# Optimization experiments

Hardware: AMD Instinct MI355X
Metric: run time of the kernel (lower is better)

The kernel has to match this reference:

```python
import jax, jax.numpy as jnp
import numpy as np

N = 50000
E = 800000
NFEAT = 128
NHID = 64
NCLASS = 40


def setup_inputs() -> dict:
    key = jax.random.key(0)
    ks = jax.random.split(key, 12)
    return {
        "x": jax.random.normal(ks[0], (N, NFEAT), dtype=jnp.float32),
        "M": jax.random.uniform(ks[1], (N, 1), dtype=jnp.float32),
        "AM": jax.random.uniform(ks[2], (N, 1), dtype=jnp.float32),
        "adj_vals": jax.random.uniform(ks[3], (E,), dtype=jnp.float32),
        "adjZ_vals": jax.random.uniform(ks[4], (E,), dtype=jnp.float32),
        "W0": jax.random.normal(ks[5], (NFEAT, NFEAT), dtype=jnp.float32) * (1.414 / np.sqrt(NFEAT)),
        "b0": jnp.zeros((NFEAT,), dtype=jnp.float32),
        "W1": jax.random.normal(ks[6], (NFEAT, NHID), dtype=jnp.float32) * (1.414 / np.sqrt(NFEAT)),
        "b1": jnp.zeros((NHID,), dtype=jnp.float32),
        "W2": jax.random.normal(ks[7], (NHID, NCLASS), dtype=jnp.float32) * (1.0 / np.sqrt(NHID)),
        "b2": jnp.zeros((NCLASS,), dtype=jnp.float32),
        "row": jax.random.randint(ks[8], (E,), 0, N, dtype=jnp.int32),
        "col": jax.random.randint(ks[9], (E,), 0, N, dtype=jnp.int32),
    }


def _spmm(vals, row, col, X, n):
    # sparse (COO) @ dense: out[r] = sum_e vals[e] * X[col[e]] for row[e]==r
    return jax.ops.segment_sum(vals[:, None] * X[col], row, num_segments=n)


def reference(x, M, AM, adj_vals, adjZ_vals, W0, b0, W1, b1, W2, b2, row, col):
    n = x.shape[0]
    # gc0: PaGConv(nfeat->nfeat) on adjZ, then ReLU (dropout is identity in eval)
    h = _spmm(adjZ_vals, row, col, M * x, n) * AM
    h = jax.nn.relu(h @ W0 + b0)
    # gc1: PaGConv(nfeat->nhid) on adjZ, then ReLU
    h = _spmm(adjZ_vals, row, col, M * h, n) * AM
    h = jax.nn.relu(h @ W1 + b1)
    # gc2: plain GConv(nhid->nclass) on adj
    h = _spmm(adj_vals, row, col, h, n)
    h = h @ W2 + b2
    return jax.nn.log_softmax(h, axis=1)
```

## Files before the change

### kernel.cpp

```cpp
#include <hip/hip_runtime.h>
#include <hip/hip_bf16.h>
#include <math.h>


typedef __attribute__((ext_vector_type(8))) short bf16x8;
typedef __attribute__((ext_vector_type(4))) float f32x4;

#define HIST_EPB_LOG 14
#define HIST_EPB 16384
#define NBINS 50176

__device__ __forceinline__ float rl_f(float v, int j) {
    return __builtin_bit_cast(float,
        __builtin_amdgcn_readlane(__builtin_bit_cast(int, v), j));
}
__device__ __forceinline__ int rl_i(int v, int j) {
    return __builtin_amdgcn_readlane(v, j);
}
__device__ __forceinline__ unsigned short f2bf(float f) {
    unsigned u = __builtin_bit_cast(unsigned, f);
    u += 0x7fffu + ((u >> 16) & 1u);
    return (unsigned short)(u >> 16);
}
__device__ __forceinline__ unsigned pack2bf(float lo, float hi) {
    return (unsigned)f2bf(lo) | ((unsigned)f2bf(hi) << 16);
}
__device__ __forceinline__ float bf_lo(unsigned u) {
    return __builtin_bit_cast(float, u << 16);
}
__device__ __forceinline__ float bf_hi(unsigned u) {
    return __builtin_bit_cast(float, u & 0xffff0000u);
}
__device__ __forceinline__ float clampf(float v) {
    return fminf(fmaxf(v, -1e30f), 1e30f);
}


__global__ void prep_wt(const float* __restrict__ W0, const float* __restrict__ W1,
                        const float* __restrict__ W2,
                        unsigned short* __restrict__ wt0, unsigned short* __restrict__ wt1,
                        unsigned short* __restrict__ wt2) {
    int idx = blockIdx.x * 256 + threadIdx.x;
    if (idx < 128 * 128) {
        int nn = idx >> 7, k = idx & 127;
        wt0[idx] = f2bf(W0[k * 128 + nn]);
    }
    idx -= 128 * 128;
    if (idx >= 0 && idx < 64 * 128) {
        int nn = idx >> 7, k = idx & 127;
        wt1[idx] = f2bf(W1[k * 64 + nn]);
    }
    idx -= 64 * 128;
    if (idx >= 0 && idx < 48 * 64) {
        int nn = idx >> 6, k = idx & 63;
        wt2[idx] = (nn < 40) ? f2bf(W2[k * 40 + nn]) : (unsigned short)0;
    }
}


template <int K, int COLS, int NTPAD, bool ABF16, bool MSCALE>
__device__ __forceinline__ void gemm_mfma_body(const void* __restrict__ Asrc,
                                               const float* __restrict__ Mv,
                                               const unsigned short* __restrict__ Wt,
                                               unsigned short* __restrict__ outp,
                                               int n, int bid, int tid) {
    constexpr int KS = K / 32;
    const int lane = tid & 63;
    const int wid = tid >> 6;
    const int m15 = lane & 15;
    const int q = lane >> 4;
    const int rA = bid * 64 + wid * 16 + m15;

    bf16x8 a[KS];
    if constexpr (ABF16) {
        const unsigned short* A = (const unsigned short*)Asrc;
#pragma unroll
        for (int ks = 0; ks < KS; ++ks) {
            uint4 z = make_uint4(0u, 0u, 0u, 0u);
            if (rA < n) z = *(const uint4*)(A + (size_t)rA * K + ks * 32 + q * 8);
            a[ks] = __builtin_bit_cast(bf16x8, z);
        }
    } else {
        const float* A = (const float*)Asrc;
        float m = 1.0f;
        if constexpr (MSCALE) { if (rA < n) m = Mv[rA]; }
#pragma unroll
        for (int ks = 0; ks < KS; ++ks) {
            float4 lo = make_float4(0.f, 0.f, 0.f, 0.f);
            float4 hi = make_float4(0.f, 0.f, 0.f, 0.f);
            if (rA < n) {
                lo = *(const float4*)(A + (size_t)rA * K + ks * 32 + q * 8);
                hi = *(const float4*)(A + (size_t)rA * K + ks * 32 + q * 8 + 4);
            }
            union { bf16x8 v; unsigned short u[8]; } pk;
            pk.u[0] = f2bf(lo.x * m); pk.u[1] = f2bf(lo.y * m);
            pk.u[2] = f2bf(lo.z * m); pk.u[3] = f2bf(lo.w * m);
            pk.u[4] = f2bf(hi.x * m); pk.u[5] = f2bf(hi.y * m);
            pk.u[6] = f2bf(hi.z * m); pk.u[7] = f2bf(hi.w * m);
            a[ks] = pk.v;
        }
    }

#pragma unroll
    for (int nt = 0; nt < NTPAD / 16; ++nt) {
        f32x4 acc = {0.f, 0.f, 0.f, 0.f};
        const int bn = nt * 16 + m15;
#pragma unroll
        for (int ks = 0; ks < KS; ++ks) {
            const uint4 z = *(const uint4*)(Wt + (size_t)bn * K + ks * 32 + q * 8);
            const bf16x8 b = __builtin_bit_cast(bf16x8, z);
            acc = __builtin_amdgcn_mfma_f32_16x16x32_bf16(a[ks], b, acc, 0, 0, 0);
        }
        const int gc = nt * 16 + m15;
#pragma unroll
        for (int rr = 0; rr < 4; ++rr) {
            const int gr = bid * 64 + wid * 16 + q * 4 + rr;
            bool ok = gr < n;
            if constexpr (NTPAD != COLS) ok = ok && (gc < COLS);
            if (ok) outp[(size_t)gr * COLS + gc] = f2bf(clampf(acc[rr]));
        }
    }
}

template <int K, int COLS, int NTPAD, bool ABF16, bool MSCALE>
__launch_bounds__(256)
__global__ void gemm_mfma(const void* __restrict__ A, const float* __restrict__ Mv,
                          const unsigned short* __restrict__ Wt,
                          unsigned short* __restrict__ out, int n) {
    gemm_mfma_body<K, COLS, NTPAD, ABF16, MSCALE>(A, Mv, Wt, out, n, blockIdx.x,
                                                  threadIdx.x);
}


__launch_bounds__(1024)
__global__ void hist_gemm0(const int* __restrict__ row,
                           unsigned short* __restrict__ cntmat,
                           unsigned short* __restrict__ lrank, int E, int NB,
                           const float* __restrict__ x, const float* __restrict__ Mv,
                           const unsigned short* __restrict__ Wt0,
                           unsigned short* __restrict__ t_buf, int n) {
    __shared__ unsigned hcnt[NBINS / 2];
    const int blk = blockIdx.x;
    const int t = threadIdx.x;
    if (blk < NB) {
        for (int i = t; i < NBINS / 2; i += 1024) hcnt[i] = 0u;
        __syncthreads();
        const int s = blk << HIST_EPB_LOG;
        const int e = min(E, s + HIST_EPB);
        for (int i = s + t; i < e; i += 1024) {
            const int r = row[i];
            const unsigned sh = (unsigned)(r & 1) << 4;
            const unsigned old = atomicAdd(&hcnt[r >> 1], 1u << sh);
            lrank[i] = (unsigned short)((old >> sh) & 0xffffu);
        }
        __syncthreads();
        unsigned* dst = (unsigned*)(cntmat + (size_t)blk * NBINS);
        for (int i = t; i < NBINS / 2; i += 1024) dst[i] = hcnt[i];
    } else {
        const int sub = t >> 8;
        gemm_mfma_body<128, 128, 128, false, true>(x, Mv, Wt0, t_buf, n,
                                                   (blk - NB) * 4 + sub, t & 255);
    }
}


__global__ void scan_sum(const unsigned short* __restrict__ cm, int* __restrict__ rp,
                         int* __restrict__ bsums, int n, int NB) {
    __shared__ int sdata[256];
    const int t = threadIdx.x;
    const int base = blockIdx.x * 1024 + t * 4;
    unsigned s0 = 0, s1 = 0, s2 = 0, s3 = 0;
    for (int b = 0; b < NB; ++b) {
        const uint2 c = *(const uint2*)&cm[(size_t)b * NBINS + base];
        s0 += c.x & 0xffffu; s1 += c.x >> 16;
        s2 += c.y & 0xffffu; s3 += c.y >> 16;
    }
    int v[4] = {(int)s0, (int)s1, (int)s2, (int)s3};
    const int tsum = v[0] + v[1] + v[2] + v[3];
    sdata[t] = tsum;
    __syncthreads();
    for (int off = 1; off < 256; off <<= 1) {
        int xv = (t >= off) ? sdata[t - off] : 0;
        __syncthreads();
        sdata[t] += xv;
        __syncthreads();
    }
    int run = sdata[t] - tsum;
    if (t == 255) bsums[blockIdx.x] = sdata[t];
#pragma unroll
    for (int i = 0; i < 4; ++i) {
        if (base + i < n) rp[base + i] = run;
        run += v[i];
    }
}


__launch_bounds__(256)
__global__ void scan_fin(const unsigned short* __restrict__ cm,
                         unsigned* __restrict__ cmabs, int* __restrict__ rp,
                         const int* __restrict__ bsums, int n, int NB, int E) {
    const int lane = threadIdx.x & 63;
    const int myblk = blockIdx.x >> 2;
    int bv = (lane < myblk) ? bsums[lane] : 0;
#pragma unroll
    for (int off = 32; off; off >>= 1) bv += __shfl_xor(bv, off);
    const int i = blockIdx.x * 256 + threadIdx.x;
    if (i < n) {
        int run = rp[i] + bv;
        rp[i] = run;
        for (int b = 0; b < NB; ++b) {
            cmabs[(size_t)b * NBINS + i] = (unsigned)run;
            run += (int)cm[(size_t)b * NBINS + i];
        }
    }
    if (blockIdx.x == 0 && threadIdx.x == 0) rp[n] = E;
}


__global__ void scatter_kernel(const int* __restrict__ row, const int* __restrict__ col,
                               const float* __restrict__ vA, const float* __restrict__ vZ,
                               const unsigned* __restrict__ cmabs,
                               const unsigned short* __restrict__ lrank,
                               float* __restrict__ packed, int E) {
    int e = blockIdx.x * blockDim.x + threadIdx.x;
    if (e >= E) return;
    const int r = row[e];
    const int pos = (int)(cmabs[(size_t)(e >> HIST_EPB_LOG) * NBINS + r]
                          + (unsigned)lrank[e]);
    float3 pk;
    pk.x = __int_as_float(col[e]);
    pk.y = vZ[e];
    pk.z = vA[e];
    *(float3*)&packed[(size_t)3 * pos] = pk;
}


__launch_bounds__(256)
__global__ void spmm128_kernel(const float* __restrict__ packed,
                               const int* __restrict__ rp, const unsigned short* __restrict__ X,
                               const float* __restrict__ AM, const float* __restrict__ Mv,
                               const float* __restrict__ bias,
                               unsigned short* __restrict__ out, int n) {
    const int lane = threadIdx.x & 63;
    const int r = (int)((blockIdx.x * (unsigned)blockDim.x + threadIdx.x) >> 6);
    if (r >= n) return;
    const int s = __builtin_amdgcn_readfirstlane(rp[r]);
    const int e = __builtin_amdgcn_readfirstlane(rp[r + 1]);

    float acc0 = 0.0f, acc1 = 0.0f;
    for (int base = s; base < e; base += 64) {
        const int nn = min(64, e - base);
        int ci = 0; float vf = 0.0f;
        if (lane < nn) {
            const float3 pk = *(const float3*)&packed[(size_t)3 * (base + lane)];
            ci = __builtin_bit_cast(int, pk.x);
            vf = pk.y;
        }
        int j = 0;
        for (; j + 16 <= nn; j += 16) {
            unsigned u[16];
#pragma unroll
            for (int q = 0; q < 16; ++q) {
                const int cq = rl_i(ci, j + q);
                u[q] = *(const unsigned*)(X + (size_t)cq * 128 + lane * 2);
            }
#pragma unroll
            for (int q = 0; q < 16; ++q) {
                const float vq = rl_f(vf, j + q);
                acc0 += vq * bf_lo(u[q]);
                acc1 += vq * bf_hi(u[q]);
            }
        }
        for (; j + 8 <= nn; j += 8) {
            unsigned u[8];
#pragma unroll
            for (int q = 0; q < 8; ++q) {
                const int cq = rl_i(ci, j + q);
                u[q] = *(const unsigned*)(X + (size_t)cq * 128 + lane * 2);
            }
#pragma unroll
            for (int q = 0; q < 8; ++q) {
                const float vq = rl_f(vf, j + q);
                acc0 += vq * bf_lo(u[q]);
                acc1 += vq * bf_hi(u[q]);
            }
        }
        for (; j < nn; ++j) {
            const int cq = rl_i(ci, j);
            const float vq = rl_f(vf, j);
            const unsigned u = *(const unsigned*)(X + (size_t)cq * 128 + lane * 2);
            acc0 += vq * bf_lo(u);
            acc1 += vq * bf_hi(u);
        }
    }

    const float am = AM[r];
    const float mr = Mv[r];
    const float o0 = fminf(fmaxf((acc0 * am + bias[2 * lane]) * mr, 0.0f), 1e30f);
    const float o1 = fminf(fmaxf((acc1 * am + bias[2 * lane + 1]) * mr, 0.0f), 1e30f);
    ((unsigned*)out)[(size_t)r * 64 + lane] = pack2bf(o0, o1);
}


__launch_bounds__(256)
__global__ void spmm64_kernel(const float* __restrict__ packed,
                              const int* __restrict__ rp, const unsigned short* __restrict__ X,
                              const float* __restrict__ AM, const float* __restrict__ bias,
                              unsigned short* __restrict__ out, int n) {
    const int lane = threadIdx.x & 63;
    const int g = lane >> 4;
    const int ls = lane & 15;
    const int r = (int)((blockIdx.x * (unsigned)blockDim.x + threadIdx.x) >> 6);
    if (r >= n) return;
    const int s = __builtin_amdgcn_readfirstlane(rp[r]);
    const int e = __builtin_amdgcn_readfirstlane(rp[r + 1]);

    float a0 = 0.0f, a1 = 0.0f, a2 = 0.0f, a3 = 0.0f;
    for (int base = s; base < e; base += 64) {
        const int nn = min(64, e - base);
        int ci = 0; float vf = 0.0f;
        if (lane < nn) {
            const float3 pk = *(const float3*)&packed[(size_t)3 * (base + lane)];
            ci = __builtin_bit_cast(int, pk.x);
            vf = pk.y;
        }
        for (int j = 0; j < nn; j += 16) {
#pragma unroll
            for (int q = 0; q < 4; ++q) {
                const int jj = j + 4 * q + g;
                const bool ok = jj < nn;
                const int idx = jj & 63;
                const int c = __shfl(ci, idx);
                const float v = __shfl(vf, idx);
                if (ok) {
                    const uint2 u = *(const uint2*)(X + (size_t)c * 64 + ls * 4);
                    a0 += v * bf_lo(u.x);
                    a1 += v * bf_hi(u.x);
                    a2 += v * bf_lo(u.y);
                    a3 += v * bf_hi(u.y);
                }
            }
        }
    }
    a0 += __shfl_xor(a0, 16); a0 += __shfl_xor(a0, 32);
    a1 += __shfl_xor(a1, 16); a1 += __shfl_xor(a1, 32);
    a2 += __shfl_xor(a2, 16); a2 += __shfl_xor(a2, 32);
    a3 += __shfl_xor(a3, 16); a3 += __shfl_xor(a3, 32);

    if (lane < 16) {
        const float am = AM[r];
        const float o0 = fminf(fmaxf(a0 * am + bias[4 * ls + 0], 0.0f), 1e30f);
        const float o1 = fminf(fmaxf(a1 * am + bias[4 * ls + 1], 0.0f), 1e30f);
        const float o2 = fminf(fmaxf(a2 * am + bias[4 * ls + 2], 0.0f), 1e30f);
        const float o3 = fminf(fmaxf(a3 * am + bias[4 * ls + 3], 0.0f), 1e30f);
        uint2 w;
        w.x = pack2bf(o0, o1);
        w.y = pack2bf(o2, o3);
        *(uint2*)((unsigned*)out + (size_t)r * 32 + ls * 2) = w;
    }
}


__launch_bounds__(256)
__global__ void spmm40_kernel(const float* __restrict__ packed,
                              const int* __restrict__ rp, const unsigned short* __restrict__ X,
                              const float* __restrict__ bias,
                              float* __restrict__ out, int n) {
    const int lane = threadIdx.x & 63;
    const int g = lane / 20;
    const int ls = lane - 20 * g;
    const bool active = g < 3;
    const int r = (int)((blockIdx.x * (unsigned)blockDim.x + threadIdx.x) >> 6);
    if (r >= n) return;
    const int s = __builtin_amdgcn_readfirstlane(rp[r]);
    const int e = __builtin_amdgcn_readfirstlane(rp[r + 1]);

    float acc0 = 0.0f, acc1 = 0.0f;
    for (int base = s; base < e; base += 64) {
        const int nn = min(64, e - base);
        int ci = 0; float vf = 0.0f;
        if (lane < nn) {
            const float3 pk = *(const float3*)&packed[(size_t)3 * (base + lane)];
            ci = __builtin_bit_cast(int, pk.x);
            vf = pk.z;
        }
        for (int j = 0; j < nn; j += 24) {
#pragma unroll
            for (int q = 0; q < 8; ++q) {
                const int jj = j + 3 * q + g;
                const bool ok = active && jj < nn;
                const int idx = jj & 63;
                const int c = __shfl(ci, idx);
                const float v = __shfl(vf, idx);
                if (ok) {
                    const unsigned u = *(const unsigned*)(X + (size_t)c * 40 + ls * 2);
                    acc0 += v * bf_lo(u);
                    acc1 += v * bf_hi(u);
                }
            }
        }
    }
    {
        const float a1 = __shfl(acc0, (lane + 20) & 63);
        const float a2 = __shfl(acc0, (lane + 40) & 63);
        const float b1 = __shfl(acc1, (lane + 20) & 63);
        const float b2 = __shfl(acc1, (lane + 40) & 63);
        acc0 += a1 + a2;
        acc1 += b1 + b2;
    }

    const bool own = lane < 20;
    const float vv0 = own ? fminf(fmaxf(acc0 + bias[2 * ls], -1e30f), 1e30f) : -INFINITY;
    const float vv1 = own ? fminf(fmaxf(acc1 + bias[2 * ls + 1], -1e30f), 1e30f) : -INFINITY;
    float mx = fmaxf(vv0, vv1);
#pragma unroll
    for (int off = 32; off > 0; off >>= 1) mx = fmaxf(mx, __shfl_xor(mx, off));
    float sum = own ? (expf(vv0 - mx) + expf(vv1 - mx)) : 0.0f;
#pragma unroll
    for (int off = 32; off > 0; off >>= 1) sum += __shfl_xor(sum, off);
    if (own) {
        const float lse = mx + logf(sum);
        *(float2*)(out + (size_t)r * 40 + ls * 2) = make_float2(vv0 - lse, vv1 - lse);
    }
}


extern "C" void kernel_launch(void* const* d_in, const int* in_sizes, int n_in,
                              void* d_out, int out_size, void* d_ws, size_t ws_size,
                              hipStream_t stream) {
    const float* x    = (const float*)d_in[0];
    const float* M    = (const float*)d_in[1];
    const float* AM   = (const float*)d_in[2];
    const float* adjv = (const float*)d_in[3];
    const float* adjZ = (const float*)d_in[4];
    const float* W0   = (const float*)d_in[5];
    const float* b0   = (const float*)d_in[6];
    const float* W1   = (const float*)d_in[7];
    const float* b1   = (const float*)d_in[8];
    const float* W2   = (const float*)d_in[9];
    const float* b2   = (const float*)d_in[10];
    const int* row    = (const int*)d_in[11];
    const int* col    = (const int*)d_in[12];
    float* out = (float*)d_out;

    const int n = in_sizes[1];
    const int E = in_sizes[3];

    float* t_f   = (float*)d_ws;
    unsigned short* t_buf = (unsigned short*)t_f;
    unsigned short* wt0 = t_buf + (size_t)n * 128;
    unsigned short* wt1 = wt0 + 128 * 128;
    unsigned short* wt2 = wt1 + 64 * 128;
    float* h_f   = t_f + (size_t)n * 128;
    unsigned short* h_buf = (unsigned short*)h_f;
    unsigned short* lrank  = (unsigned short*)h_f;
    unsigned short* cntmat = lrank + (size_t)E;
    unsigned* cmabs = (unsigned*)(cntmat + (size_t)64 * NBINS);
    int* rp      = (int*)(h_f + (size_t)n * 128);
    int* bsums   = rp + (n + 1);
    float* packed = (float*)(bsums + 64);

    const int NB = (E + HIST_EPB - 1) >> HIST_EPB_LOG;
    const int gemmBlocks = (n + 63) / 64;
    const int gemmB4 = (gemmBlocks + 3) / 4;

    prep_wt<<<(128 * 128 + 64 * 128 + 48 * 64 + 255) / 256, 256, 0, stream>>>(
        W0, W1, W2, wt0, wt1, wt2);

    hist_gemm0<<<NB + gemmB4, 1024, 0, stream>>>(row, cntmat, lrank, E, NB,
                                                 x, M, wt0, t_buf, n);

    const int nblk = (n + 1023) >> 10;
    scan_sum<<<nblk, 256, 0, stream>>>(cntmat, rp, bsums, n, NB);
    scan_fin<<<(n + 255) / 256, 256, 0, stream>>>(cntmat, cmabs, rp, bsums, n, NB, E);
    scatter_kernel<<<(E + 255) / 256, 256, 0, stream>>>(row, col, adjv, adjZ,
                                                        cmabs, lrank, packed, E);

    const int spmmBlocks = (n + 3) / 4;

    spmm128_kernel<<<spmmBlocks, 256, 0, stream>>>(packed, rp, t_buf, AM, M, b0, h_buf, n);
    gemm_mfma<128, 64, 64, true, false><<<gemmBlocks, 256, 0, stream>>>(h_buf, nullptr, wt1,
                                                                        t_buf, n);
    spmm64_kernel<<<spmmBlocks, 256, 0, stream>>>(packed, rp, t_buf, AM, b1, h_buf, n);
    gemm_mfma<64, 40, 48, true, false><<<gemmBlocks, 256, 0, stream>>>(h_buf, nullptr, wt2,
                                                                       t_buf, n);
    spmm40_kernel<<<spmmBlocks, 256, 0, stream>>>(packed, rp, t_buf, b2, out, n);
}
```

Baseline: 278.3 us.

## Merge scan kernels with decoupled lookback, split packed edges, enlarge hist blocks

```diff
diff --git a/kernel.cpp b/kernel.cpp
--- a/kernel.cpp
+++ b/kernel.cpp
@@ -6,9 +6,11 @@
 typedef __attribute__((ext_vector_type(8))) short bf16x8;
 typedef __attribute__((ext_vector_type(4))) float f32x4;
 
-#define HIST_EPB_LOG 14
-#define HIST_EPB 16384
+#define HIST_EPB_LOG 15
+#define HIST_EPB 32768
 #define NBINS 50176
+#define NBMAX 32
+#define SCAN_BLOCKS 196
 
 __device__ __forceinline__ float rl_f(float v, int j) {
     return __builtin_bit_cast(float,
@@ -139,11 +141,13 @@
                            const float* __restrict__ x, const float* __restrict__ Mv,
                            const unsigned short* __restrict__ Wt0,
                            unsigned short* __restrict__ t_buf, int n) {
-    __shared__ unsigned hcnt[NBINS / 2];
+    __shared__ __align__(16) unsigned hcnt[NBINS / 2];
     const int blk = blockIdx.x;
     const int t = threadIdx.x;
     if (blk < NB) {
-        for (int i = t; i < NBINS / 2; i += 1024) hcnt[i] = 0u;
+        uint4* h4 = (uint4*)hcnt;
+        const uint4 z4 = make_uint4(0u, 0u, 0u, 0u);
+        for (int i = t; i < NBINS / 8; i += 1024) h4[i] = z4;
         __syncthreads();
         const int s = blk << HIST_EPB_LOG;
         const int e = min(E, s + HIST_EPB);
@@ -154,8 +158,8 @@
             lrank[i] = (unsigned short)((old >> sh) & 0xffffu);
         }
         __syncthreads();
-        unsigned* dst = (unsigned*)(cntmat + (size_t)blk * NBINS);
-        for (int i = t; i < NBINS / 2; i += 1024) dst[i] = hcnt[i];
+        uint4* dst = (uint4*)(cntmat + (size_t)blk * NBINS);
+        for (int i = t; i < NBINS / 8; i += 1024) dst[i] = h4[i];
     } else {
         const int sub = t >> 8;
         gemm_mfma_body<128, 128, 128, false, true>(x, Mv, Wt0, t_buf, n,
@@ -164,56 +168,57 @@
 }
 
 
-__global__ void scan_sum(const unsigned short* __restrict__ cm, int* __restrict__ rp,
-                         int* __restrict__ bsums, int n, int NB) {
-    __shared__ int sdata[256];
+__launch_bounds__(256)
+__global__ void scan_one(const unsigned short* __restrict__ cm,
+                         unsigned* __restrict__ cmabs, int* __restrict__ rp,
+                         unsigned long long* __restrict__ gpub,
+                         int n, int NB, int E) {
+    __shared__ int sd[256];
+    const int g = blockIdx.x;
     const int t = threadIdx.x;
-    const int base = blockIdx.x * 1024 + t * 4;
-    unsigned s0 = 0, s1 = 0, s2 = 0, s3 = 0;
-    for (int b = 0; b < NB; ++b) {
-        const uint2 c = *(const uint2*)&cm[(size_t)b * NBINS + base];
-        s0 += c.x & 0xffffu; s1 += c.x >> 16;
-        s2 += c.y & 0xffffu; s3 += c.y >> 16;
-    }
-    int v[4] = {(int)s0, (int)s1, (int)s2, (int)s3};
-    const int tsum = v[0] + v[1] + v[2] + v[3];
-    sdata[t] = tsum;
+    const int bin = g * 256 + t;
+
+    unsigned tot = 0;
+    for (int b = 0; b < NB; ++b) tot += cm[(size_t)b * NBINS + bin];
+
+    sd[t] = (int)tot;
     __syncthreads();
     for (int off = 1; off < 256; off <<= 1) {
-        int xv = (t >= off) ? sdata[t - off] : 0;
+        int xv = (t >= off) ? sd[t - off] : 0;
         __syncthreads();
-        sdata[t] += xv;
+        sd[t] += xv;
         __syncthreads();
     }
-    int run = sdata[t] - tsum;
-    if (t == 255) bsums[blockIdx.x] = sdata[t];
-#pragma unroll
-    for (int i = 0; i < 4; ++i) {
-        if (base + i < n) rp[base + i] = run;
-        run += v[i];
-    }
-}
-
-
-__launch_bounds__(256)
-__global__ void scan_fin(const unsigned short* __restrict__ cm,
-                         unsigned* __restrict__ cmabs, int* __restrict__ rp,
-                         const int* __restrict__ bsums, int n, int NB, int E) {
-    const int lane = threadIdx.x & 63;
-    const int myblk = blockIdx.x >> 2;
-    int bv = (lane < myblk) ? bsums[lane] : 0;
-#pragma unroll
-    for (int off = 32; off; off >>= 1) bv += __shfl_xor(bv, off);
-    const int i = blockIdx.x * 256 + threadIdx.x;
-    if (i < n) {
-        int run = rp[i] + bv;
-        rp[i] = run;
-        for (int b = 0; b < NB; ++b) {
-            cmabs[(size_t)b * NBINS + i] = (unsigned)run;
-            run += (int)cm[(size_t)b * NBINS + i];
-        }
-    }
-    if (blockIdx.x == 0 && threadIdx.x == 0) rp[n] = E;
+    const int excl = sd[t] - (int)tot;
+    const int gtot = sd[255];
+    __syncthreads();
+
+    if (t == 0)
+        atomicExch(&gpub[g], (1ULL << 32) | (unsigned long long)(unsigned)gtot);
+
+    int my = 0;
+    for (int p = t; p < g; p += 256) {
+        unsigned long long v;
+        do { v = atomicAdd(&gpub[p], 0ULL); } while ((v >> 32) == 0ULL);
+        my += (int)(unsigned)v;
+    }
+    sd[t] = my;
+    __syncthreads();
+    for (int off = 128; off > 0; off >>= 1) {
+        if (t < off) sd[t] += sd[t + off];
+        __syncthreads();
+    }
+    const int base = sd[0];
+
+    const int rpf = base + excl;
+    if (bin < n) rp[bin] = rpf;
+    if (g == SCAN_BLOCKS - 1 && t == 255) rp[n] = E;
+
+    int run = rpf;
+    for (int b = 0; b < NB; ++b) {
+        cmabs[(size_t)b * NBINS + bin] = (unsigned)run;
+        run += (int)cm[(size_t)b * NBINS + bin];
+    }
 }
 
 
@@ -221,22 +226,22 @@
                                const float* __restrict__ vA, const float* __restrict__ vZ,
                                const unsigned* __restrict__ cmabs,
                                const unsigned short* __restrict__ lrank,
-                               float* __restrict__ packed, int E) {
+                               uint2* __restrict__ cz, float* __restrict__ va, int E) {
     int e = blockIdx.x * blockDim.x + threadIdx.x;
     if (e >= E) return;
     const int r = row[e];
     const int pos = (int)(cmabs[(size_t)(e >> HIST_EPB_LOG) * NBINS + r]
                           + (unsigned)lrank[e]);
-    float3 pk;
-    pk.x = __int_as_float(col[e]);
-    pk.y = vZ[e];
-    pk.z = vA[e];
-    *(float3*)&packed[(size_t)3 * pos] = pk;
+    uint2 pk;
+    pk.x = (unsigned)col[e];
+    pk.y = __builtin_bit_cast(unsigned, vZ[e]);
+    cz[pos] = pk;
+    va[pos] = vA[e];
 }
 
 
 __launch_bounds__(256)
-__global__ void spmm128_kernel(const float* __restrict__ packed,
+__global__ void spmm128_kernel(const uint2* __restrict__ cz,
                                const int* __restrict__ rp, const unsigned short* __restrict__ X,
                                const float* __restrict__ AM, const float* __restrict__ Mv,
                                const float* __restrict__ bias,
@@ -252,9 +257,9 @@
         const int nn = min(64, e - base);
         int ci = 0; float vf = 0.0f;
         if (lane < nn) {
-            const float3 pk = *(const float3*)&packed[(size_t)3 * (base + lane)];
-            ci = __builtin_bit_cast(int, pk.x);
-            vf = pk.y;
+            const uint2 pk = cz[base + lane];
+            ci = (int)pk.x;
+            vf = __builtin_bit_cast(float, pk.y);
         }
         int j = 0;
         for (; j + 16 <= nn; j += 16) {
@@ -303,7 +308,7 @@
 
 
 __launch_bounds__(256)
-__global__ void spmm64_kernel(const float* __restrict__ packed,
+__global__ void spmm64_kernel(const uint2* __restrict__ cz,
                               const int* __restrict__ rp, const unsigned short* __restrict__ X,
                               const float* __restrict__ AM, const float* __restrict__ bias,
                               unsigned short* __restrict__ out, int n) {
@@ -320,9 +325,9 @@
         const int nn = min(64, e - base);
         int ci = 0; float vf = 0.0f;
         if (lane < nn) {
-            const float3 pk = *(const float3*)&packed[(size_t)3 * (base + lane)];
-            ci = __builtin_bit_cast(int, pk.x);
-            vf = pk.y;
+            const uint2 pk = cz[base + lane];
+            ci = (int)pk.x;
+            vf = __builtin_bit_cast(float, pk.y);
         }
         for (int j = 0; j < nn; j += 16) {
 #pragma unroll
@@ -362,7 +367,8 @@
 
 
 __launch_bounds__(256)
-__global__ void spmm40_kernel(const float* __restrict__ packed,
+__global__ void spmm40_kernel(const uint2* __restrict__ cz,
+                              const float* __restrict__ va,
                               const int* __restrict__ rp, const unsigned short* __restrict__ X,
                               const float* __restrict__ bias,
                               float* __restrict__ out, int n) {
@@ -380,9 +386,8 @@
         const int nn = min(64, e - base);
         int ci = 0; float vf = 0.0f;
         if (lane < nn) {
-            const float3 pk = *(const float3*)&packed[(size_t)3 * (base + lane)];
-            ci = __builtin_bit_cast(int, pk.x);
-            vf = pk.z;
+            ci = (int)cz[base + lane].x;
+            vf = va[base + lane];
         }
         for (int j = 0; j < nn; j += 24) {
 #pragma unroll
@@ -455,34 +460,35 @@
     unsigned short* h_buf = (unsigned short*)h_f;
     unsigned short* lrank  = (unsigned short*)h_f;
     unsigned short* cntmat = lrank + (size_t)E;
-    unsigned* cmabs = (unsigned*)(cntmat + (size_t)64 * NBINS);
+    unsigned* cmabs = (unsigned*)(cntmat + (size_t)NBMAX * NBINS);
     int* rp      = (int*)(h_f + (size_t)n * 128);
-    int* bsums   = rp + (n + 1);
-    float* packed = (float*)(bsums + 64);
+    unsigned long long* gpub = (unsigned long long*)(rp + n + 2);
+    uint2* cz    = (uint2*)(gpub + 256);
+    float* va    = (float*)(cz + (size_t)E);
 
     const int NB = (E + HIST_EPB - 1) >> HIST_EPB_LOG;
     const int gemmBlocks = (n + 63) / 64;
     const int gemmB4 = (gemmBlocks + 3) / 4;
 
+    hipMemsetAsync(gpub, 0, 256 * sizeof(unsigned long long), stream);
     prep_wt<<<(128 * 128 + 64 * 128 + 48 * 64 + 255) / 256, 256, 0, stream>>>(
         W0, W1, W2, wt0, wt1, wt2);
 
     hist_gemm0<<<NB + gemmB4, 1024, 0, stream>>>(row, cntmat, lrank, E, NB,
                                                  x, M, wt0, t_buf, n);
 
-    const int nblk = (n + 1023) >> 10;
-    scan_sum<<<nblk, 256, 0, stream>>>(cntmat, rp, bsums, n, NB);
-    scan_fin<<<(n + 255) / 256, 256, 0, stream>>>(cntmat, cmabs, rp, bsums, n, NB, E);
+    scan_one<<<SCAN_BLOCKS, 256, 0, stream>>>(cntmat, cmabs, rp, gpub, n, NB, E);
+
     scatter_kernel<<<(E + 255) / 256, 256, 0, stream>>>(row, col, adjv, adjZ,
-                                                        cmabs, lrank, packed, E);
+                                                        cmabs, lrank, cz, va, E);
 
     const int spmmBlocks = (n + 3) / 4;
 
-    spmm128_kernel<<<spmmBlocks, 256, 0, stream>>>(packed, rp, t_buf, AM, M, b0, h_buf, n);
+    spmm128_kernel<<<spmmBlocks, 256, 0, stream>>>(cz, rp, t_buf, AM, M, b0, h_buf, n);
     gemm_mfma<128, 64, 64, true, false><<<gemmBlocks, 256, 0, stream>>>(h_buf, nullptr, wt1,
                                                                         t_buf, n);
-    spmm64_kernel<<<spmmBlocks, 256, 0, stream>>>(packed, rp, t_buf, AM, b1, h_buf, n);
+    spmm64_kernel<<<spmmBlocks, 256, 0, stream>>>(cz, rp, t_buf, AM, b1, h_buf, n);
     gemm_mfma<64, 40, 48, true, false><<<gemmBlocks, 256, 0, stream>>>(h_buf, nullptr, wt2,
                                                                        t_buf, n);
-    spmm40_kernel<<<spmmBlocks, 256, 0, stream>>>(packed, rp, t_buf, b2, out, n);
-}
+    spmm40_kernel<<<spmmBlocks, 256, 0, stream>>>(cz, va, rp, t_buf, b2, out, n);
+}
```

Result: faster. 269.9 us (-3.0%).
